# Kernel tuning notes

Hardware: AMD Instinct MI355X
Metric: run time of the kernel (lower is better)

Reference implementation:

```python
import jax, jax.numpy as jnp
import numpy as np

N_EMBD = 512
HEAD_SIZE = 64
B, T = 256, 256


def setup_inputs() -> dict:
    key = jax.random.key(0)
    ks = jax.random.split(key, 7)
    s = 1.0 / np.sqrt(N_EMBD)
    return {
        "x": jax.random.normal(ks[0], (B, T, N_EMBD), dtype=jnp.float32),
        "Wk": jax.random.uniform(ks[1], (N_EMBD, HEAD_SIZE), jnp.float32, -s, s),
        "bk": jax.random.uniform(ks[2], (HEAD_SIZE,), jnp.float32, -s, s),
        "Wq": jax.random.uniform(ks[3], (N_EMBD, HEAD_SIZE), jnp.float32, -s, s),
        "bq": jax.random.uniform(ks[4], (HEAD_SIZE,), jnp.float32, -s, s),
        "Wv": jax.random.uniform(ks[5], (N_EMBD, HEAD_SIZE), jnp.float32, -s, s),
        "bv": jax.random.uniform(ks[6], (HEAD_SIZE,), jnp.float32, -s, s),
    }


def reference(x, Wk, bk, Wq, bq, Wv, bv):
    # Single-head causal self-attention (dropout = identity in eval mode).
    Bq, Tq, C = x.shape
    k = x @ Wk + bk        # [B, T, H]
    q = x @ Wq + bq        # [B, T, H]
    v = x @ Wv + bv        # [B, T, H]
    scale = 1.0 / jnp.sqrt(jnp.asarray(k.shape[-1], x.dtype))
    scores = jnp.einsum('bth,bsh->bts', q, k) * scale  # [B, T, T]
    causal = jnp.tril(jnp.ones((Tq, Tq), dtype=bool))
    scores = jnp.where(causal, scores, -jnp.inf)
    attn = jax.nn.softmax(scores, axis=-1)
    return jnp.einsum('bts,bsh->bth', attn, v)  # [B, T, H]
```

## Files before the change

kernel.cpp:

```cpp
#include <hip/hip_runtime.h>
#include <stdint.h>

typedef __attribute__((ext_vector_type(8))) short bf16x8;
typedef __attribute__((ext_vector_type(4))) float f32x4;

#if __has_builtin(__builtin_amdgcn_exp2f)
#define EXP2F(x) __builtin_amdgcn_exp2f(x)
#else
#define EXP2F(x) exp2f(x)
#endif

__device__ __forceinline__ short f2bf(float f) {
    union { float f; uint32_t u; } c; c.f = f;
    return (short)((c.u + 0x7fffu + ((c.u >> 16) & 1u)) >> 16);
}

typedef __attribute__((address_space(1))) void gvoid;
typedef __attribute__((address_space(3))) void lvoid;
__device__ __forceinline__ void async_cp16(const void* g, void* l) {
    __builtin_amdgcn_global_load_lds((gvoid*)g, (lvoid*)l, 16, 0, 0);
}

__global__ void prep_kernel(const float* __restrict__ Wk, const float* __restrict__ bk,
                            const float* __restrict__ Wq, const float* __restrict__ bq,
                            const float* __restrict__ Wv, const float* __restrict__ bv,
                            short* __restrict__ Wt2g, float* __restrict__ bcat) {
    const int col = blockIdx.x;
    const float* W; const float* bb; int c0;
    if (col < 64)       { W = Wk; bb = bk; c0 = col; }
    else if (col < 128) { W = Wq; bb = bq; c0 = col - 64; }
    else                { W = Wv; bb = bv; c0 = col - 128; }
    for (int c = threadIdx.x; c < 512; c += blockDim.x)
        Wt2g[(c >> 5) * (192 * 32) + col * 32 + (c & 31)] = f2bf(W[(size_t)c * 64 + c0]);
    if (threadIdx.x == 0) bcat[col] = bb[c0];
}

#define PSTR 40

__global__ __launch_bounds__(1024, 4) void fused_kernel(
    const float* __restrict__ x, const short* __restrict__ Wt2g,
    const float* __restrict__ bcat, float* __restrict__ out) {
    extern __shared__ __align__(16) char smem[];

    const int tid = threadIdx.x;
    const int wave = tid >> 6, lane = tid & 63;
    const int quad = lane >> 4, l16 = lane & 15;
    const int b = blockIdx.x;
    const int t = wave;

    f32x4 acc[12];
#pragma unroll
    for (int i = 0; i < 12; i++) acc[i] = (f32x4){0.f, 0.f, 0.f, 0.f};

    const int xr = lane >> 3;
    const int xsl = lane & 7;

#define STAGE_X(kc, bufp)                                                           \
    for (int g = 0; g < 2; g++) {                                                   \
        const int i = wave + g * 16;                                                \
        const int r = i * 8 + xr;                                                   \
        const int s = xsl ^ ((r & 3) << 1);                                         \
        async_cp16(x + ((size_t)b * 256 + r) * 512 + (kc) * 32 + s * 4,             \
                   smem + (bufp) * 32768 + i * 1024);                               \
    }
#define STAGE_W(kc, bufp)                                                           \
    if (wave < 12) {                                                                \
        async_cp16(Wt2g + (size_t)(kc) * 6144 + wave * 512 + lane * 8,              \
                   smem + 65536 + (bufp) * 12288 + wave * 1024);                    \
    }

    STAGE_X(0, 0)
    STAGE_W(0, 0)
    __syncthreads();

    const int axoff = (quad ^ (l16 & 3)) * 8;
    const int arow = t * 16 + l16;
    for (int kc = 0; kc < 16; kc++) {
        const int buf = kc & 1;
        if (kc < 15) { STAGE_X(kc + 1, buf ^ 1) STAGE_W(kc + 1, buf ^ 1) }
        const float* xa = (const float*)(smem + buf * 32768) + arow * 32 + axoff;
        f32x4 u0 = *(const f32x4*)xa, u1 = *(const f32x4*)(xa + 4);
        bf16x8 a;
#pragma unroll
        for (int i = 0; i < 4; i++) { a[i] = f2bf(u0[i]); a[4 + i] = f2bf(u1[i]); }
        const short* wb = (const short*)(smem + 65536 + buf * 12288);
#pragma unroll
        for (int nt = 0; nt < 12; nt++) {
            bf16x8 bfrag = *(const bf16x8*)&wb[(nt * 16 + l16) * 32 + quad * 8];
            acc[nt] = __builtin_amdgcn_mfma_f32_16x16x32_bf16(a, bfrag, acc[nt], 0, 0, 0);
        }
        __syncthreads();
    }

    short* Ks  = (short*)smem;
    short* Qs  = (short*)(smem + 32768);
    short* Vts = (short*)(smem + 65536);
    short* Ps  = (short*)(smem + 98304);
#pragma unroll
    for (int nt = 0; nt < 12; nt++) {
        const int col = nt * 16 + l16;
        const float bias = bcat[col];
        const int h = col & 63;
#pragma unroll
        for (int r = 0; r < 4; r++) {
            const short v = f2bf(acc[nt][r] + bias);
            const int row = t * 16 + quad * 4 + r;
            if (nt < 4)
                Ks[row * 64 + (((h >> 3) ^ (row & 7)) << 3) + (h & 7)] = v;
            else if (nt < 8)
                Qs[row * 64 + (((h >> 3) ^ (row & 7)) << 3) + (h & 7)] = v;
            else
                Vts[h * 256 + (((row >> 3) ^ (h & 7)) << 3) + (row & 7)] = v;
        }
    }
    __syncthreads();

    const float sc2 = 0.125f * 1.44269504088896340736f;
    short* myP = Ps + wave * (16 * PSTR);

    const int qrow = t * 16 + l16;
    const int sw = l16 & 7;
    bf16x8 qf0 = *(const bf16x8*)&Qs[qrow * 64 + ((quad ^ sw) << 3)];
    bf16x8 qf1 = *(const bf16x8*)&Qs[qrow * 64 + (((4 + quad) ^ sw) << 3)];

    f32x4 St[16];
#pragma unroll
    for (int i = 0; i < 16; i++) St[i] = (f32x4){0.f, 0.f, 0.f, 0.f};
#pragma unroll
    for (int nt = 0; nt < 16; nt++) if (nt <= t) {
        const int krow = nt * 16 + l16;
        bf16x8 kf0 = *(const bf16x8*)&Ks[krow * 64 + ((quad ^ sw) << 3)];
        bf16x8 kf1 = *(const bf16x8*)&Ks[krow * 64 + (((4 + quad) ^ sw) << 3)];
        St[nt] = __builtin_amdgcn_mfma_f32_16x16x32_bf16(qf0, kf0, St[nt], 0, 0, 0);
        St[nt] = __builtin_amdgcn_mfma_f32_16x16x32_bf16(qf1, kf1, St[nt], 0, 0, 0);
    }

    const int rowq = t * 16 + quad * 4;
    float mx[4], ls[4];
#pragma unroll
    for (int r = 0; r < 4; r++) mx[r] = -3.0e38f;
#pragma unroll
    for (int nt = 0; nt < 16; nt++) if (nt <= t) {
        const int cs = nt * 16 + l16;
#pragma unroll
        for (int r = 0; r < 4; r++) {
            float s = (cs <= rowq + r) ? St[nt][r] * sc2 : -3.0e38f;
            St[nt][r] = s;
            mx[r] = fmaxf(mx[r], s);
        }
    }
#pragma unroll
    for (int d = 1; d < 16; d <<= 1)
#pragma unroll
        for (int r = 0; r < 4; r++)
            mx[r] = fmaxf(mx[r], __shfl_xor(mx[r], d, 64));
#pragma unroll
    for (int r = 0; r < 4; r++) ls[r] = 0.f;
#pragma unroll
    for (int nt = 0; nt < 16; nt++) if (nt <= t) {
#pragma unroll
        for (int r = 0; r < 4; r++) {
            float p = EXP2F(St[nt][r] - mx[r]);
            St[nt][r] = p;
            ls[r] += p;
        }
    }
#pragma unroll
    for (int d = 1; d < 16; d <<= 1)
#pragma unroll
        for (int r = 0; r < 4; r++)
            ls[r] += __shfl_xor(ls[r], d, 64);

    f32x4 O[4];
#pragma unroll
    for (int i = 0; i < 4; i++) O[i] = (f32x4){0.f, 0.f, 0.f, 0.f};
    const int nch = (t + 2) >> 1;
#pragma unroll
    for (int c2 = 0; c2 < 8; c2++) if (c2 < nch) {
#pragma unroll
        for (int t2i = 0; t2i < 2; t2i++) {
            const int nt = c2 * 2 + t2i;
#pragma unroll
            for (int r = 0; r < 4; r++)
                myP[(quad * 4 + r) * PSTR + t2i * 16 + l16] = f2bf(St[nt][r]);
        }
        bf16x8 pf = *(const bf16x8*)&myP[l16 * PSTR + quad * 8];
#pragma unroll
        for (int ht = 0; ht < 4; ht++) {
            const int h = ht * 16 + l16;
            bf16x8 vf = *(const bf16x8*)&Vts[h * 256 + (((c2 * 4 + quad) ^ (h & 7)) << 3)];
            O[ht] = __builtin_amdgcn_mfma_f32_16x16x32_bf16(pf, vf, O[ht], 0, 0, 0);
        }
    }

    float rls[4];
#pragma unroll
    for (int r = 0; r < 4; r++) rls[r] = 1.0f / ls[r];
#pragma unroll
    for (int ht = 0; ht < 4; ht++)
#pragma unroll
        for (int r = 0; r < 4; r++)
            out[((size_t)b * 256 + rowq + r) * 64 + ht * 16 + l16] = O[ht][r] * rls[r];
#undef STAGE_X
#undef STAGE_W
}

extern "C" void kernel_launch(void* const* d_in, const int* in_sizes, int n_in,
                              void* d_out, int out_size, void* d_ws, size_t ws_size,
                              hipStream_t stream) {
    const float* x  = (const float*)d_in[0];
    const float* Wk = (const float*)d_in[1];
    const float* bk = (const float*)d_in[2];
    const float* Wq = (const float*)d_in[3];
    const float* bq = (const float*)d_in[4];
    const float* Wv = (const float*)d_in[5];
    const float* bv = (const float*)d_in[6];
    float* out = (float*)d_out;

    char* ws = (char*)d_ws;
    short* Wt2g = (short*)(ws);
    float* bcat = (float*)(ws + 196608);

    const int smem_bytes = 118784;
    (void)hipFuncSetAttribute((const void*)fused_kernel,
                              hipFuncAttributeMaxDynamicSharedMemorySize, smem_bytes);

    prep_kernel<<<192, 256, 0, stream>>>(Wk, bk, Wq, bq, Wv, bv, Wt2g, bcat);
    fused_kernel<<<256, 1024, smem_bytes, stream>>>(x, Wt2g, bcat, out);
}
```

Before: 217.1 us.

## Split each batch into two query-half blocks with redundant K/V projection

Each batch now runs as two 512-thread blocks, one per half of the query rows, giving 512 blocks instead of 256. The second half recomputes K/V for all rows it needs, and the first half loads only the first half of x. W fragments are now read straight from global/L2 instead of being staged in LDS. Q is routed through the per-wave P buffer, which cuts LDS use so more blocks can be resident. The cost is extra projection work and x traffic for the upper half, plus global-memory latency on the weight loads.

```diff
diff --git a/kernel.cpp b/kernel.cpp
--- a/kernel.cpp
+++ b/kernel.cpp
@@ -37,7 +37,7 @@
 
 #define PSTR 40
 
-__global__ __launch_bounds__(1024, 4) void fused_kernel(
+__global__ __launch_bounds__(512, 4) void fused_kernel(
     const float* __restrict__ x, const short* __restrict__ Wt2g,
     const float* __restrict__ bcat, float* __restrict__ out) {
     extern __shared__ __align__(16) char smem[];
@@ -45,102 +45,133 @@
     const int tid = threadIdx.x;
     const int wave = tid >> 6, lane = tid & 63;
     const int quad = lane >> 4, l16 = lane & 15;
-    const int b = blockIdx.x;
-    const int t = wave;
-
-    f32x4 acc[12];
-#pragma unroll
-    for (int i = 0; i < 12; i++) acc[i] = (f32x4){0.f, 0.f, 0.f, 0.f};
+    const int b = blockIdx.x >> 1;
+    const int jh = blockIdx.x & 1;
+    const int tq = jh * 8 + wave;
+
+    f32x4 acc_kv[2][8];
+    f32x4 acc_q[4];
+#pragma unroll
+    for (int m = 0; m < 2; m++)
+#pragma unroll
+        for (int i = 0; i < 8; i++) acc_kv[m][i] = (f32x4){0.f, 0.f, 0.f, 0.f};
+#pragma unroll
+    for (int i = 0; i < 4; i++) acc_q[i] = (f32x4){0.f, 0.f, 0.f, 0.f};
 
     const int xr = lane >> 3;
     const int xsl = lane & 7;
+    const int glim = 2 * (jh + 1);
 
 #define STAGE_X(kc, bufp)                                                           \
-    for (int g = 0; g < 2; g++) {                                                   \
-        const int i = wave + g * 16;                                                \
+    for (int g = 0; g < 4; g++) if (g < glim) {                                     \
+        const int i = wave + g * 8;                                                 \
         const int r = i * 8 + xr;                                                   \
         const int s = xsl ^ ((r & 3) << 1);                                         \
         async_cp16(x + ((size_t)b * 256 + r) * 512 + (kc) * 32 + s * 4,             \
                    smem + (bufp) * 32768 + i * 1024);                               \
     }
-#define STAGE_W(kc, bufp)                                                           \
-    if (wave < 12) {                                                                \
-        async_cp16(Wt2g + (size_t)(kc) * 6144 + wave * 512 + lane * 8,              \
-                   smem + 65536 + (bufp) * 12288 + wave * 1024);                    \
-    }
 
     STAGE_X(0, 0)
-    STAGE_W(0, 0)
     __syncthreads();
 
-    const int axoff = (quad ^ (l16 & 3)) * 8;
-    const int arow = t * 16 + l16;
     for (int kc = 0; kc < 16; kc++) {
         const int buf = kc & 1;
-        if (kc < 15) { STAGE_X(kc + 1, buf ^ 1) STAGE_W(kc + 1, buf ^ 1) }
-        const float* xa = (const float*)(smem + buf * 32768) + arow * 32 + axoff;
-        f32x4 u0 = *(const f32x4*)xa, u1 = *(const f32x4*)(xa + 4);
-        bf16x8 a;
-#pragma unroll
-        for (int i = 0; i < 4; i++) { a[i] = f2bf(u0[i]); a[4 + i] = f2bf(u1[i]); }
-        const short* wb = (const short*)(smem + 65536 + buf * 12288);
+        if (kc < 15) { STAGE_X(kc + 1, buf ^ 1) }
+        bf16x8 a[2];
+        {
+            const int arow = wave * 16 + l16;
+            const float* xa = (const float*)(smem + buf * 32768) +
+                              arow * 32 + ((quad ^ (arow & 3)) << 3);
+            f32x4 u0 = *(const f32x4*)xa, u1 = *(const f32x4*)(xa + 4);
+#pragma unroll
+            for (int i = 0; i < 4; i++) { a[0][i] = f2bf(u0[i]); a[0][4 + i] = f2bf(u1[i]); }
+        }
+        if (jh) {
+            const int arow = (wave + 8) * 16 + l16;
+            const float* xa = (const float*)(smem + buf * 32768) +
+                              arow * 32 + ((quad ^ (arow & 3)) << 3);
+            f32x4 u0 = *(const f32x4*)xa, u1 = *(const f32x4*)(xa + 4);
+#pragma unroll
+            for (int i = 0; i < 4; i++) { a[1][i] = f2bf(u0[i]); a[1][4 + i] = f2bf(u1[i]); }
+        }
+        const short* wkc = Wt2g + (size_t)kc * 6144 + l16 * 32 + quad * 8;
 #pragma unroll
         for (int nt = 0; nt < 12; nt++) {
-            bf16x8 bfrag = *(const bf16x8*)&wb[(nt * 16 + l16) * 32 + quad * 8];
-            acc[nt] = __builtin_amdgcn_mfma_f32_16x16x32_bf16(a, bfrag, acc[nt], 0, 0, 0);
+            bf16x8 bfrag = *(const bf16x8*)(wkc + nt * 512);
+            if (nt < 4) {
+                acc_kv[0][nt] = __builtin_amdgcn_mfma_f32_16x16x32_bf16(a[0], bfrag, acc_kv[0][nt], 0, 0, 0);
+                if (jh) acc_kv[1][nt] = __builtin_amdgcn_mfma_f32_16x16x32_bf16(a[1], bfrag, acc_kv[1][nt], 0, 0, 0);
+            } else if (nt < 8) {
+                acc_q[nt - 4] = __builtin_amdgcn_mfma_f32_16x16x32_bf16(a[jh], bfrag, acc_q[nt - 4], 0, 0, 0);
+            } else {
+                acc_kv[0][nt - 4] = __builtin_amdgcn_mfma_f32_16x16x32_bf16(a[0], bfrag, acc_kv[0][nt - 4], 0, 0, 0);
+                if (jh) acc_kv[1][nt - 4] = __builtin_amdgcn_mfma_f32_16x16x32_bf16(a[1], bfrag, acc_kv[1][nt - 4], 0, 0, 0);
+            }
         }
         __syncthreads();
     }
 
     short* Ks  = (short*)smem;
-    short* Qs  = (short*)(smem + 32768);
-    short* Vts = (short*)(smem + 65536);
-    short* Ps  = (short*)(smem + 98304);
-#pragma unroll
-    for (int nt = 0; nt < 12; nt++) {
-        const int col = nt * 16 + l16;
-        const float bias = bcat[col];
-        const int h = col & 63;
-#pragma unroll
-        for (int r = 0; r < 4; r++) {
-            const short v = f2bf(acc[nt][r] + bias);
-            const int row = t * 16 + quad * 4 + r;
-            if (nt < 4)
-                Ks[row * 64 + (((h >> 3) ^ (row & 7)) << 3) + (h & 7)] = v;
-            else if (nt < 8)
-                Qs[row * 64 + (((h >> 3) ^ (row & 7)) << 3) + (h & 7)] = v;
-            else
-                Vts[h * 256 + (((row >> 3) ^ (h & 7)) << 3) + (row & 7)] = v;
-        }
+    short* Vts = (short*)(smem + 32768);
+    short* Ps  = (short*)(smem + 65536);
+    const int mlim = jh ? 2 : 1;
+#pragma unroll
+    for (int m = 0; m < 2; m++) if (m < mlim) {
+        const int rowb = (wave + m * 8) * 16 + quad * 4;
+#pragma unroll
+        for (int nt8 = 0; nt8 < 8; nt8++) {
+            const int h = (nt8 & 3) * 16 + l16;
+            const float bias = bcat[(nt8 < 4 ? 0 : 128) + h];
+#pragma unroll
+            for (int r = 0; r < 4; r++) {
+                const short v = f2bf(acc_kv[m][nt8][r] + bias);
+                const int row = rowb + r;
+                if (nt8 < 4)
+                    Ks[row * 64 + (((h >> 3) ^ (row & 7)) << 3) + (h & 7)] = v;
+                else
+                    Vts[h * 256 + (((row >> 3) ^ (h & 7)) << 3) + (row & 7)] = v;
+            }
+        }
+    }
+
+    short* myP = Ps + wave * (16 * PSTR);
+    bf16x8 qf0, qf1;
+#pragma unroll
+    for (int half = 0; half < 2; half++) {
+#pragma unroll
+        for (int nt2 = 0; nt2 < 2; nt2++) {
+            const int qi = half * 2 + nt2;
+            const float bias = bcat[64 + qi * 16 + l16];
+#pragma unroll
+            for (int r = 0; r < 4; r++)
+                myP[(quad * 4 + r) * PSTR + nt2 * 16 + l16] = f2bf(acc_q[qi][r] + bias);
+        }
+        if (half == 0) qf0 = *(const bf16x8*)&myP[l16 * PSTR + quad * 8];
+        else           qf1 = *(const bf16x8*)&myP[l16 * PSTR + quad * 8];
     }
     __syncthreads();
 
     const float sc2 = 0.125f * 1.44269504088896340736f;
-    short* myP = Ps + wave * (16 * PSTR);
-
-    const int qrow = t * 16 + l16;
     const int sw = l16 & 7;
-    bf16x8 qf0 = *(const bf16x8*)&Qs[qrow * 64 + ((quad ^ sw) << 3)];
-    bf16x8 qf1 = *(const bf16x8*)&Qs[qrow * 64 + (((4 + quad) ^ sw) << 3)];
 
     f32x4 St[16];
 #pragma unroll
     for (int i = 0; i < 16; i++) St[i] = (f32x4){0.f, 0.f, 0.f, 0.f};
 #pragma unroll
-    for (int nt = 0; nt < 16; nt++) if (nt <= t) {
+    for (int nt = 0; nt < 16; nt++) if (nt <= tq) {
         const int krow = nt * 16 + l16;
-        bf16x8 kf0 = *(const bf16x8*)&Ks[krow * 64 + ((quad ^ sw) << 3)];
-        bf16x8 kf1 = *(const bf16x8*)&Ks[krow * 64 + (((4 + quad) ^ sw) << 3)];
+        bf16x8 kf0 = *(const bf16x8*)&Ks[krow * 64 + ((quad ^ (krow & 7)) << 3)];
+        bf16x8 kf1 = *(const bf16x8*)&Ks[krow * 64 + (((4 + quad) ^ (krow & 7)) << 3)];
         St[nt] = __builtin_amdgcn_mfma_f32_16x16x32_bf16(qf0, kf0, St[nt], 0, 0, 0);
         St[nt] = __builtin_amdgcn_mfma_f32_16x16x32_bf16(qf1, kf1, St[nt], 0, 0, 0);
     }
 
-    const int rowq = t * 16 + quad * 4;
+    const int rowq = tq * 16 + quad * 4;
     float mx[4], ls[4];
 #pragma unroll
     for (int r = 0; r < 4; r++) mx[r] = -3.0e38f;
 #pragma unroll
-    for (int nt = 0; nt < 16; nt++) if (nt <= t) {
+    for (int nt = 0; nt < 16; nt++) if (nt <= tq) {
         const int cs = nt * 16 + l16;
 #pragma unroll
         for (int r = 0; r < 4; r++) {
@@ -157,7 +188,7 @@
 #pragma unroll
     for (int r = 0; r < 4; r++) ls[r] = 0.f;
 #pragma unroll
-    for (int nt = 0; nt < 16; nt++) if (nt <= t) {
+    for (int nt = 0; nt < 16; nt++) if (nt <= tq) {
 #pragma unroll
         for (int r = 0; r < 4; r++) {
             float p = EXP2F(St[nt][r] - mx[r]);
@@ -174,7 +205,7 @@
     f32x4 O[4];
 #pragma unroll
     for (int i = 0; i < 4; i++) O[i] = (f32x4){0.f, 0.f, 0.f, 0.f};
-    const int nch = (t + 2) >> 1;
+    const int nch = (tq + 2) >> 1;
 #pragma unroll
     for (int c2 = 0; c2 < 8; c2++) if (c2 < nch) {
 #pragma unroll
@@ -202,7 +233,6 @@
         for (int r = 0; r < 4; r++)
             out[((size_t)b * 256 + rowq + r) * 64 + ht * 16 + l16] = O[ht][r] * rls[r];
 #undef STAGE_X
-#undef STAGE_W
 }
 
 extern "C" void kernel_launch(void* const* d_in, const int* in_sizes, int n_in,
@@ -221,10 +251,10 @@
     short* Wt2g = (short*)(ws);
     float* bcat = (float*)(ws + 196608);
 
-    const int smem_bytes = 118784;
+    const int smem_bytes = 75776;
     (void)hipFuncSetAttribute((const void*)fused_kernel,
                               hipFuncAttributeMaxDynamicSharedMemorySize, smem_bytes);
 
     prep_kernel<<<192, 256, 0, stream>>>(Wk, bk, Wq, bq, Wv, bv, Wt2g, bcat);
-    fused_kernel<<<256, 1024, smem_bytes, stream>>>(x, Wt2g, bcat, out);
-}
+    fused_kernel<<<512, 512, smem_bytes, stream>>>(x, Wt2g, bcat, out);
+}
```

Result: slower. 278.3 us (+28.2%).

## Switch projection GEMM to 32x32 MFMA with per-wave x staging and direct W loads

Applied to the files above, without the earlier changes.

The QKV projection now uses 32x32x16 MFMA tiles, with each wave owning a 32-row by 96-column output block. Each wave stages its own x rows into a private LDS region, so the per-k-step __syncthreads are removed. Weight fragments are read straight from global memory (L2) in a new prepacked layout instead of being staged through LDS. This trades block-wide barriers and LDS weight traffic for more global and L2 weight reads and a larger LDS allocation (128 KB).

```diff
diff --git a/kernel.cpp b/kernel.cpp
--- a/kernel.cpp
+++ b/kernel.cpp
@@ -3,6 +3,7 @@
 
 typedef __attribute__((ext_vector_type(8))) short bf16x8;
 typedef __attribute__((ext_vector_type(4))) float f32x4;
+typedef __attribute__((ext_vector_type(16))) float f32x16;
 
 #if __has_builtin(__builtin_amdgcn_exp2f)
 #define EXP2F(x) __builtin_amdgcn_exp2f(x)
@@ -10,6 +11,8 @@
 #define EXP2F(x) exp2f(x)
 #endif
 
+#define WAITV0() __builtin_amdgcn_s_waitcnt(0x0F70)
+
 __device__ __forceinline__ short f2bf(float f) {
     union { float f; uint32_t u; } c; c.f = f;
     return (short)((c.u + 0x7fffu + ((c.u >> 16) & 1u)) >> 16);
@@ -24,101 +27,110 @@
 __global__ void prep_kernel(const float* __restrict__ Wk, const float* __restrict__ bk,
                             const float* __restrict__ Wq, const float* __restrict__ bq,
                             const float* __restrict__ Wv, const float* __restrict__ bv,
-                            short* __restrict__ Wt2g, float* __restrict__ bcat) {
+                            short* __restrict__ Wt3, float* __restrict__ bcat) {
     const int col = blockIdx.x;
     const float* W; const float* bb; int c0;
     if (col < 64)       { W = Wk; bb = bk; c0 = col; }
     else if (col < 128) { W = Wq; bb = bq; c0 = col - 64; }
     else                { W = Wv; bb = bv; c0 = col - 128; }
-    for (int c = threadIdx.x; c < 512; c += blockDim.x)
-        Wt2g[(c >> 5) * (192 * 32) + col * 32 + (c & 31)] = f2bf(W[(size_t)c * 64 + c0]);
+    const int n32 = col >> 5, cc = col & 31;
+    for (int c = threadIdx.x; c < 512; c += blockDim.x) {
+        const int kstep = c >> 4, khh = (c >> 3) & 1, i = c & 7;
+        Wt3[(size_t)(kstep * 6 + n32) * 512 + cc * 16 + khh * 8 + i] = f2bf(W[(size_t)c * 64 + c0]);
+    }
     if (threadIdx.x == 0) bcat[col] = bb[c0];
 }
 
 #define PSTR 40
 
 __global__ __launch_bounds__(1024, 4) void fused_kernel(
-    const float* __restrict__ x, const short* __restrict__ Wt2g,
+    const float* __restrict__ x, const short* __restrict__ Wt3,
     const float* __restrict__ bcat, float* __restrict__ out) {
     extern __shared__ __align__(16) char smem[];
 
     const int tid = threadIdx.x;
     const int wave = tid >> 6, lane = tid & 63;
     const int quad = lane >> 4, l16 = lane & 15;
+    const int l32 = lane & 31, kh = lane >> 5;
     const int b = blockIdx.x;
-    const int t = wave;
-
-    f32x4 acc[12];
-#pragma unroll
-    for (int i = 0; i < 12; i++) acc[i] = (f32x4){0.f, 0.f, 0.f, 0.f};
-
-    const int xr = lane >> 3;
-    const int xsl = lane & 7;
-
-#define STAGE_X(kc, bufp)                                                           \
-    for (int g = 0; g < 2; g++) {                                                   \
-        const int i = wave + g * 16;                                                \
-        const int r = i * 8 + xr;                                                   \
-        const int s = xsl ^ ((r & 3) << 1);                                         \
-        async_cp16(x + ((size_t)b * 256 + r) * 512 + (kc) * 32 + s * 4,             \
-                   smem + (bufp) * 32768 + i * 1024);                               \
-    }
-#define STAGE_W(kc, bufp)                                                           \
-    if (wave < 12) {                                                                \
-        async_cp16(Wt2g + (size_t)(kc) * 6144 + wave * 512 + lane * 8,              \
-                   smem + 65536 + (bufp) * 12288 + wave * 1024);                    \
-    }
+    const int m32 = wave >> 1, ng = wave & 1;
+
+    f32x16 acc[3];
+#pragma unroll
+    for (int t = 0; t < 3; t++)
+#pragma unroll
+        for (int i = 0; i < 16; i++) acc[t][i] = 0.f;
+
+    char* sbase = smem + wave * 8192;
+    const int srow = lane >> 3;
+    const int ssl = (lane & 7) ^ srow;
+
+#define STAGE_X(kc, bufp)                                                            \
+    for (int g = 0; g < 4; g++)                                                      \
+        async_cp16(x + ((size_t)b * 256 + m32 * 32 + g * 8 + srow) * 512 +           \
+                       (kc) * 32 + ssl * 4,                                          \
+                   sbase + (bufp) * 4096 + g * 1024);
 
     STAGE_X(0, 0)
-    STAGE_W(0, 0)
-    __syncthreads();
-
-    const int axoff = (quad ^ (l16 & 3)) * 8;
-    const int arow = t * 16 + l16;
+
+#pragma unroll
     for (int kc = 0; kc < 16; kc++) {
         const int buf = kc & 1;
-        if (kc < 15) { STAGE_X(kc + 1, buf ^ 1) STAGE_W(kc + 1, buf ^ 1) }
-        const float* xa = (const float*)(smem + buf * 32768) + arow * 32 + axoff;
-        f32x4 u0 = *(const f32x4*)xa, u1 = *(const f32x4*)(xa + 4);
-        bf16x8 a;
-#pragma unroll
-        for (int i = 0; i < 4; i++) { a[i] = f2bf(u0[i]); a[4 + i] = f2bf(u1[i]); }
-        const short* wb = (const short*)(smem + 65536 + buf * 12288);
-#pragma unroll
-        for (int nt = 0; nt < 12; nt++) {
-            bf16x8 bfrag = *(const bf16x8*)&wb[(nt * 16 + l16) * 32 + quad * 8];
-            acc[nt] = __builtin_amdgcn_mfma_f32_16x16x32_bf16(a, bfrag, acc[nt], 0, 0, 0);
-        }
-        __syncthreads();
-    }
+        WAITV0();
+        bf16x8 wf[2][3];
+#pragma unroll
+        for (int ks = 0; ks < 2; ks++)
+#pragma unroll
+            for (int t = 0; t < 3; t++) {
+                const int n32 = t * 2 + ng;
+                wf[ks][t] = *(const bf16x8*)&Wt3[(size_t)((kc * 2 + ks) * 6 + n32) * 512 +
+                                                 l32 * 16 + kh * 8];
+            }
+        bf16x8 a[2];
+#pragma unroll
+        for (int ks = 0; ks < 2; ks++) {
+            const float* ap = (const float*)(sbase + buf * 4096 + l32 * 128);
+            const int s0 = (ks * 4 + kh * 2 + 0) ^ (l32 & 7);
+            const int s1 = (ks * 4 + kh * 2 + 1) ^ (l32 & 7);
+            f32x4 u0 = *(const f32x4*)(ap + s0 * 4);
+            f32x4 u1 = *(const f32x4*)(ap + s1 * 4);
+#pragma unroll
+            for (int i = 0; i < 4; i++) { a[ks][i] = f2bf(u0[i]); a[ks][4 + i] = f2bf(u1[i]); }
+        }
+        if (kc < 15) { STAGE_X(kc + 1, buf ^ 1) }
+#pragma unroll
+        for (int ks = 0; ks < 2; ks++)
+#pragma unroll
+            for (int t = 0; t < 3; t++)
+                acc[t] = __builtin_amdgcn_mfma_f32_32x32x16_bf16(a[ks], wf[ks][t], acc[t], 0, 0, 0);
+    }
+
+    __syncthreads();
 
     short* Ks  = (short*)smem;
     short* Qs  = (short*)(smem + 32768);
     short* Vts = (short*)(smem + 65536);
     short* Ps  = (short*)(smem + 98304);
 #pragma unroll
-    for (int nt = 0; nt < 12; nt++) {
-        const int col = nt * 16 + l16;
-        const float bias = bcat[col];
-        const int h = col & 63;
-#pragma unroll
-        for (int r = 0; r < 4; r++) {
-            const short v = f2bf(acc[nt][r] + bias);
-            const int row = t * 16 + quad * 4 + r;
-            if (nt < 4)
-                Ks[row * 64 + (((h >> 3) ^ (row & 7)) << 3) + (h & 7)] = v;
-            else if (nt < 8)
-                Qs[row * 64 + (((h >> 3) ^ (row & 7)) << 3) + (h & 7)] = v;
-            else
-                Vts[h * 256 + (((row >> 3) ^ (h & 7)) << 3) + (row & 7)] = v;
+    for (int t = 0; t < 3; t++) {
+        const int h = ng * 32 + l32;
+        const float bias = bcat[t * 64 + h];
+#pragma unroll
+        for (int reg = 0; reg < 16; reg++) {
+            const int row = m32 * 32 + (reg & 3) + 8 * (reg >> 2) + 4 * kh;
+            const short v = f2bf(acc[t][reg] + bias);
+            if (t == 0)      Ks[row * 64 + (((h >> 3) ^ (row & 7)) << 3) + (h & 7)] = v;
+            else if (t == 1) Qs[row * 64 + (((h >> 3) ^ (row & 7)) << 3) + (h & 7)] = v;
+            else             Vts[h * 256 + (((row >> 3) ^ (h & 7)) << 3) + (row & 7)] = v;
         }
     }
     __syncthreads();
 
     const float sc2 = 0.125f * 1.44269504088896340736f;
     short* myP = Ps + wave * (16 * PSTR);
-
-    const int qrow = t * 16 + l16;
+    const int tq = wave;
+
+    const int qrow = tq * 16 + l16;
     const int sw = l16 & 7;
     bf16x8 qf0 = *(const bf16x8*)&Qs[qrow * 64 + ((quad ^ sw) << 3)];
     bf16x8 qf1 = *(const bf16x8*)&Qs[qrow * 64 + (((4 + quad) ^ sw) << 3)];
@@ -127,20 +139,20 @@
 #pragma unroll
     for (int i = 0; i < 16; i++) St[i] = (f32x4){0.f, 0.f, 0.f, 0.f};
 #pragma unroll
-    for (int nt = 0; nt < 16; nt++) if (nt <= t) {
+    for (int nt = 0; nt < 16; nt++) if (nt <= tq) {
         const int krow = nt * 16 + l16;
-        bf16x8 kf0 = *(const bf16x8*)&Ks[krow * 64 + ((quad ^ sw) << 3)];
-        bf16x8 kf1 = *(const bf16x8*)&Ks[krow * 64 + (((4 + quad) ^ sw) << 3)];
+        bf16x8 kf0 = *(const bf16x8*)&Ks[krow * 64 + ((quad ^ (krow & 7)) << 3)];
+        bf16x8 kf1 = *(const bf16x8*)&Ks[krow * 64 + (((4 + quad) ^ (krow & 7)) << 3)];
         St[nt] = __builtin_amdgcn_mfma_f32_16x16x32_bf16(qf0, kf0, St[nt], 0, 0, 0);
         St[nt] = __builtin_amdgcn_mfma_f32_16x16x32_bf16(qf1, kf1, St[nt], 0, 0, 0);
     }
 
-    const int rowq = t * 16 + quad * 4;
+    const int rowq = tq * 16 + quad * 4;
     float mx[4], ls[4];
 #pragma unroll
     for (int r = 0; r < 4; r++) mx[r] = -3.0e38f;
 #pragma unroll
-    for (int nt = 0; nt < 16; nt++) if (nt <= t) {
+    for (int nt = 0; nt < 16; nt++) if (nt <= tq) {
         const int cs = nt * 16 + l16;
 #pragma unroll
         for (int r = 0; r < 4; r++) {
@@ -157,7 +169,7 @@
 #pragma unroll
     for (int r = 0; r < 4; r++) ls[r] = 0.f;
 #pragma unroll
-    for (int nt = 0; nt < 16; nt++) if (nt <= t) {
+    for (int nt = 0; nt < 16; nt++) if (nt <= tq) {
 #pragma unroll
         for (int r = 0; r < 4; r++) {
             float p = EXP2F(St[nt][r] - mx[r]);
@@ -174,7 +186,7 @@
     f32x4 O[4];
 #pragma unroll
     for (int i = 0; i < 4; i++) O[i] = (f32x4){0.f, 0.f, 0.f, 0.f};
-    const int nch = (t + 2) >> 1;
+    const int nch = (tq + 2) >> 1;
 #pragma unroll
     for (int c2 = 0; c2 < 8; c2++) if (c2 < nch) {
 #pragma unroll
@@ -202,7 +214,6 @@
         for (int r = 0; r < 4; r++)
             out[((size_t)b * 256 + rowq + r) * 64 + ht * 16 + l16] = O[ht][r] * rls[r];
 #undef STAGE_X
-#undef STAGE_W
 }
 
 extern "C" void kernel_launch(void* const* d_in, const int* in_sizes, int n_in,
@@ -218,13 +229,13 @@
     float* out = (float*)d_out;
 
     char* ws = (char*)d_ws;
-    short* Wt2g = (short*)(ws);
+    short* Wt3  = (short*)(ws);
     float* bcat = (float*)(ws + 196608);
 
-    const int smem_bytes = 118784;
+    const int smem_bytes = 131072;
     (void)hipFuncSetAttribute((const void*)fused_kernel,
                               hipFuncAttributeMaxDynamicSharedMemorySize, smem_bytes);
 
-    prep_kernel<<<192, 256, 0, stream>>>(Wk, bk, Wq, bq, Wv, bv, Wt2g, bcat);
-    fused_kernel<<<256, 1024, smem_bytes, stream>>>(x, Wt2g, bcat, out);
-}
+    prep_kernel<<<192, 256, 0, stream>>>(Wk, bk, Wq, bq, Wv, bv, Wt3, bcat);
+    fused_kernel<<<256, 1024, smem_bytes, stream>>>(x, Wt3, bcat, out);
+}
```

After: 221.8 us. +2.2%, slower.
